# Optimization experiments

Measured on AMD Instinct MI355X. Metric: run time of the kernel, lower is better.

Reference implementation:

```python
import jax, jax.numpy as jnp
import numpy as np

N_STATES = 96
B = 524288
L = 12  # 1 root + 5 level-2 + 6 level-3 labels (ffsc)
EPS = 1e-8


def _make_legal_state():
    # Deterministic legal-state matrix: col 0 = root bit, cols 1:6 one-hot
    # level-2 class, cols 6:12 level-3 binary attributes.
    S = np.zeros((N_STATES, L), dtype=np.float32)
    for s in range(N_STATES):
        S[s, 0] = s % 2
        S[s, 1 + (s // 2) % 5] = 1.0
        bits = (s // 10) % 64
        for b in range(6):
            S[s, 6 + b] = (bits >> b) & 1
    return jnp.asarray(S)


def setup_inputs() -> dict:
    key = jax.random.key(0)
    kf, ky = jax.random.split(key)
    f = jax.random.normal(kf, (B, L), dtype=jnp.float32)
    y = jax.random.randint(ky, (B, L), 0, 2, dtype=jnp.int64)
    S = _make_legal_state()  # [N_STATES, L] binary legal-state matrix (hexG[0])
    return {"f": f, "y": y, "S": S}


def _fidelity(p, g):
    # 1 - (sqrt(p*g+eps) + sqrt((1-p)*(1-g)+eps)), averaged over all elems;
    # matches both Fidelity_Loss_binary and Multi_Fidelity_Loss (no mask).
    return jnp.mean(1.0 - (jnp.sqrt(p * g + EPS) + jnp.sqrt((1.0 - p) * (1.0 - g) + EPS)))


def reference(f, y, S):
    yf = y.astype(jnp.float32)
    # potential = S @ f.T : [N_STATES, B]
    potential = jnp.matmul(S, f.T)
    # stable exp-normalize over states (columnwise max subtract)
    J = jnp.exp(potential - jnp.max(potential, axis=0, keepdims=True))
    z = jnp.sum(J, axis=0)  # [B]
    # per-column masked sum loop -> single matmul: pMargin[b,i] = sum_{s: S[s,i]>0} J[s,b] / z[b]
    mask = (S > 0).astype(f.dtype)  # [N_STATES, L]
    pMargin = jnp.matmul(J.T, mask) / z[:, None]  # [B, L]
    p1, p2, p3 = pMargin[:, 0], pMargin[:, 1:6], pMargin[:, 6:]
    g1, g2, g3 = yf[:, 0], yf[:, 1:6], yf[:, 6:]
    loss1 = _fidelity(p1, g1)
    loss2 = _fidelity(p2, g2)
    loss3 = _fidelity(p3, g3)
    all_loss = jnp.stack([loss1, loss2, loss3])
    return all_loss, pMargin
```

## Files before the change

### kernel.cpp

```cpp
#include <hip/hip_runtime.h>

#define EPSF 1e-8f
#define BLOCK 256
#define ROWS 256
#define CHUNK_F (ROWS * 12)
#define LSTR 13

__device__ __forceinline__ float fid_term(float p, float g) {
    return 1.0f - sqrtf(p * g + EPSF) - sqrtf((1.0f - p) * (1.0f - g) + EPSF);
}

__global__ __launch_bounds__(BLOCK) void ploss_kernel(
    const float* __restrict__ f, const int* __restrict__ y,
    float* __restrict__ partials, float* __restrict__ pM,
    int n, int nChunks)
{
    __shared__ __align__(16) float lbuf[ROWS * LSTR];
    const int t = threadIdx.x;
    const int c = blockIdx.x;
    float l1 = 0.f, l2 = 0.f, l3 = 0.f;

    if (c < nChunks) {
        const int vrows = min(ROWS, n - c * ROWS);
        const int vfl = vrows * 12;
        const size_t cbase = (size_t)c * CHUNK_F;

        const float4* f4 = (const float4*)(f + cbase);
        const int4*   y4 = (const int4*)(y + cbase);
        int4 yv[3];
        float4 fv[3];
        #pragma unroll
        for (int k = 0; k < 3; ++k) {
            const int s = k * 256 + t;
            if (4 * s < vfl) { fv[k] = f4[s]; yv[k] = y4[s]; }
            else             { yv[k] = make_int4(0, 0, 0, 0); }
        }
        #pragma unroll
        for (int k = 0; k < 3; ++k) {
            const int s = k * 256 + t;
            if (4 * s < vfl) {
                float* dst = &lbuf[(s / 3) * LSTR + (s % 3) * 4];
                dst[0] = fv[k].x; dst[1] = fv[k].y; dst[2] = fv[k].z; dst[3] = fv[k].w;
            }
        }
        __syncthreads();

        const float a  = lbuf[t * LSTR + 0];
        const float B0 = lbuf[t * LSTR + 1], B1 = lbuf[t * LSTR + 2],
                    B2 = lbuf[t * LSTR + 3], B3 = lbuf[t * LSTR + 4],
                    B4 = lbuf[t * LSTR + 5];
        const float c0 = lbuf[t * LSTR + 6], c1 = lbuf[t * LSTR + 7],
                    c2 = lbuf[t * LSTR + 8], c3 = lbuf[t * LSTR + 9];
        __syncthreads();

        const float C1 = c0, C2 = c1, C3 = c0 + c1, C4 = c2, C5 = c0 + c2,
                    C6 = c1 + c2, C7 = c0 + c1 + c2, C8 = c3, C9 = c0 + c3;
        float maxC = fmaxf(0.f, C1);
        maxC = fmaxf(maxC, fmaxf(C2, C3));
        maxC = fmaxf(maxC, fmaxf(C4, C5));
        maxC = fmaxf(maxC, fmaxf(C6, C7));
        maxC = fmaxf(maxC, fmaxf(C8, C9));
        const float EC0 = __expf(0.f - maxC), EC1 = __expf(C1 - maxC),
                    EC2 = __expf(C2 - maxC), EC3 = __expf(C3 - maxC),
                    EC4 = __expf(C4 - maxC), EC5 = __expf(C5 - maxC),
                    EC6 = __expf(C6 - maxC), EC7 = __expf(C7 - maxC),
                    EC8 = __expf(C8 - maxC), EC9 = __expf(C9 - maxC);
        const float ST8 = ((EC0 + EC1) + (EC2 + EC3)) +
                          ((EC4 + EC5) + (EC6 + EC7)) + EC8;
        const float E9  = EC9;

        const float maxB = fmaxf(fmaxf(B0, B1), fmaxf(B2, fmaxf(B3, B4)));
        const float EB0 = __expf(B0 - maxB), EB1 = __expf(B1 - maxB),
                    EB2 = __expf(B2 - maxB), EB3 = __expf(B3 - maxB),
                    EB4 = __expf(B4 - maxB);
        const float SB  = (EB0 + EB1) + (EB2 + EB3) + EB4;
        const float SB3 = EB0 + EB1 + EB2;

        const float invD = 1.0f / (ST8 * SB + E9 * SB3);
        const float TF   = ST8 + E9;
        const float U0 = (EC1 + EC3) + (EC5 + EC7);
        const float U1 = (EC2 + EC3) + (EC6 + EC7);
        const float U2 = (EC4 + EC5) + (EC6 + EC7);
        const float E9SB3 = E9 * SB3;

        float4 p0, p1, p2;
        p0.x = 1.0f / (1.0f + __expf(-a));
        p0.y = EB0 * TF  * invD;
        p0.z = EB1 * TF  * invD;
        p0.w = EB2 * TF  * invD;
        p1.x = EB3 * ST8 * invD;
        p1.y = EB4 * ST8 * invD;
        p1.z = (SB * U0 + E9SB3) * invD;
        p1.w = SB * U1 * invD;
        p2.x = SB * U2 * invD;
        p2.y = (SB * EC8 + E9SB3) * invD;
        p2.z = 0.f;
        p2.w = 0.f;

        float4* pb = (float4*)lbuf;
        pb[t * 3 + 0] = p0;
        pb[t * 3 + 1] = p1;
        pb[t * 3 + 2] = p2;
        __syncthreads();

        float4* pM4 = (float4*)(pM + cbase);
        #pragma unroll
        for (int k = 0; k < 3; ++k) {
            const int s = k * 256 + t;
            if (4 * s < vfl) {
                const float4 pv = pb[s];
                pM4[s] = pv;
                const int colbase = 4 * (s % 3);
                const float pe[4] = {pv.x, pv.y, pv.z, pv.w};
                const int   ye[4] = {yv[k].x, yv[k].y, yv[k].z, yv[k].w};
                #pragma unroll
                for (int j = 0; j < 4; ++j) {
                    const float fd = fid_term(pe[j], (float)ye[j]);
                    const int col = colbase + j;
                    if (col == 0)     l1 += fd;
                    else if (col < 6) l2 += fd;
                    else              l3 += fd;
                }
            }
        }
    }

    #pragma unroll
    for (int off = 32; off > 0; off >>= 1) {
        l1 += __shfl_down(l1, off);
        l2 += __shfl_down(l2, off);
        l3 += __shfl_down(l3, off);
    }
    __syncthreads();
    const int lane = t & 63;
    const int wid  = t >> 6;
    if (lane == 0) { lbuf[wid] = l1; lbuf[4 + wid] = l2; lbuf[8 + wid] = l3; }
    __syncthreads();
    if (t == 0) {
        partials[blockIdx.x]                 = (lbuf[0] + lbuf[1]) + (lbuf[2] + lbuf[3]);
        partials[gridDim.x + blockIdx.x]     = (lbuf[4] + lbuf[5]) + (lbuf[6] + lbuf[7]);
        partials[2 * gridDim.x + blockIdx.x] = (lbuf[8] + lbuf[9]) + (lbuf[10] + lbuf[11]);
    }
}

__global__ __launch_bounds__(BLOCK) void loss_reduce_kernel(
    const float* __restrict__ partials, float* __restrict__ loss_out,
    int nb, float fn)
{
    const int t = threadIdx.x;
    float s1 = 0.f, s2 = 0.f, s3 = 0.f;
    for (int i = t; i < nb; i += BLOCK) {
        s1 += partials[i];
        s2 += partials[nb + i];
        s3 += partials[2 * nb + i];
    }
    #pragma unroll
    for (int off = 32; off > 0; off >>= 1) {
        s1 += __shfl_down(s1, off);
        s2 += __shfl_down(s2, off);
        s3 += __shfl_down(s3, off);
    }
    __shared__ float sm[12];
    const int lane = t & 63, wid = t >> 6;
    if (lane == 0) { sm[wid] = s1; sm[4 + wid] = s2; sm[8 + wid] = s3; }
    __syncthreads();
    if (t == 0) {
        loss_out[0] = ((sm[0] + sm[1]) + (sm[2] + sm[3])) / fn;
        loss_out[1] = ((sm[4] + sm[5]) + (sm[6] + sm[7])) / (5.0f * fn);
        loss_out[2] = ((sm[8] + sm[9]) + (sm[10] + sm[11])) / (6.0f * fn);
    }
}

extern "C" void kernel_launch(void* const* d_in, const int* in_sizes, int n_in,
                              void* d_out, int out_size, void* d_ws, size_t ws_size,
                              hipStream_t stream) {
    const float* f = (const float*)d_in[0];
    const int*   y = (const int*)d_in[1];
    float* out = (float*)d_out;
    float* ws  = (float*)d_ws;
    const int n = in_sizes[0] / 12;

    const int nChunks = (n + ROWS - 1) / ROWS;
    ploss_kernel<<<nChunks, BLOCK, 0, stream>>>(f, y, ws, out + 3, n, nChunks);
    loss_reduce_kernel<<<1, BLOCK, 0, stream>>>(ws, out, nChunks, (float)n);
}
```

Before: 105.1 us.

## Process two chunks per block with register prefetch of the next chunk

```diff
diff --git a/kernel.cpp b/kernel.cpp
--- a/kernel.cpp
+++ b/kernel.cpp
@@ -5,42 +5,66 @@
 #define ROWS 256
 #define CHUNK_F (ROWS * 12)
 #define LSTR 13
+#define CPB 2
 
 __device__ __forceinline__ float fid_term(float p, float g) {
     return 1.0f - sqrtf(p * g + EPSF) - sqrtf((1.0f - p) * (1.0f - g) + EPSF);
 }
 
-__global__ __launch_bounds__(BLOCK) void ploss_kernel(
+__global__ __launch_bounds__(BLOCK, 4) void ploss_kernel(
     const float* __restrict__ f, const int* __restrict__ y,
     float* __restrict__ partials, float* __restrict__ pM,
     int n, int nChunks)
 {
     __shared__ __align__(16) float lbuf[ROWS * LSTR];
     const int t = threadIdx.x;
-    const int c = blockIdx.x;
     float l1 = 0.f, l2 = 0.f, l3 = 0.f;
 
-    if (c < nChunks) {
-        const int vrows = min(ROWS, n - c * ROWS);
-        const int vfl = vrows * 12;
-        const size_t cbase = (size_t)c * CHUNK_F;
-
-        const float4* f4 = (const float4*)(f + cbase);
-        const int4*   y4 = (const int4*)(y + cbase);
-        int4 yv[3];
-        float4 fv[3];
+    const int chunk0 = blockIdx.x * CPB;
+
+    float4 fv[3];
+    int4   yv[3];
+    if (chunk0 < nChunks) {
+        const int vfl = min(ROWS, n - chunk0 * ROWS) * 12;
+        const float4* f4 = (const float4*)(f + (size_t)chunk0 * CHUNK_F);
+        const int4*   y4 = (const int4*)(y + (size_t)chunk0 * CHUNK_F);
         #pragma unroll
         for (int k = 0; k < 3; ++k) {
             const int s = k * 256 + t;
             if (4 * s < vfl) { fv[k] = f4[s]; yv[k] = y4[s]; }
             else             { yv[k] = make_int4(0, 0, 0, 0); }
         }
+    }
+
+    #pragma unroll
+    for (int it = 0; it < CPB; ++it) {
+        const int cc = chunk0 + it;
+        if (cc >= nChunks) break;
+        const int vrows = min(ROWS, n - cc * ROWS);
+        const int vfl = vrows * 12;
+
         #pragma unroll
         for (int k = 0; k < 3; ++k) {
             const int s = k * 256 + t;
             if (4 * s < vfl) {
                 float* dst = &lbuf[(s / 3) * LSTR + (s % 3) * 4];
                 dst[0] = fv[k].x; dst[1] = fv[k].y; dst[2] = fv[k].z; dst[3] = fv[k].w;
+            }
+        }
+
+        float4 fv2[3];
+        int4   yv2[3];
+        const int  cn = cc + 1;
+        const bool havenext = (it + 1 < CPB) && (cn < nChunks);
+        if (havenext) {
+            const int vfln = min(ROWS, n - cn * ROWS) * 12;
+            const float4* f4n = (const float4*)(f + (size_t)cn * CHUNK_F);
+            const int4*   y4n = (const int4*)(y + (size_t)cn * CHUNK_F);
+            #pragma unroll
+            for (int k = 0; k < 3; ++k) {
+                const int s = k * 256 + t;
+                if (4 * s < vfln) { fv2[k] = f4n[s]; yv2[k] = y4n[s]; }
+                else              { yv2[k] = make_int4(0, 0, 0, 0); }
             }
         }
         __syncthreads();
@@ -103,7 +127,7 @@
         pb[t * 3 + 2] = p2;
         __syncthreads();
 
-        float4* pM4 = (float4*)(pM + cbase);
+        float4* pM4 = (float4*)(pM + (size_t)cc * CHUNK_F);
         #pragma unroll
         for (int k = 0; k < 3; ++k) {
             const int s = k * 256 + t;
@@ -123,6 +147,12 @@
                 }
             }
         }
+        __syncthreads();
+
+        if (havenext) {
+            #pragma unroll
+            for (int k = 0; k < 3; ++k) { fv[k] = fv2[k]; yv[k] = yv2[k]; }
+        }
     }
 
     #pragma unroll
@@ -131,7 +161,6 @@
         l2 += __shfl_down(l2, off);
         l3 += __shfl_down(l3, off);
     }
-    __syncthreads();
     const int lane = t & 63;
     const int wid  = t >> 6;
     if (lane == 0) { lbuf[wid] = l1; lbuf[4 + wid] = l2; lbuf[8 + wid] = l3; }
@@ -181,6 +210,7 @@
     const int n = in_sizes[0] / 12;
 
     const int nChunks = (n + ROWS - 1) / ROWS;
-    ploss_kernel<<<nChunks, BLOCK, 0, stream>>>(f, y, ws, out + 3, n, nChunks);
-    loss_reduce_kernel<<<1, BLOCK, 0, stream>>>(ws, out, nChunks, (float)n);
-}
+    const int nb      = (nChunks + CPB - 1) / CPB;
+    ploss_kernel<<<nb, BLOCK, 0, stream>>>(f, y, ws, out + 3, n, nChunks);
+    loss_reduce_kernel<<<1, BLOCK, 0, stream>>>(ws, out, nb, (float)n);
+}
```

New measurement: 104.6 us. Within noise of the previous version (-0.5%).
